# Performance work log

Hardware: AMD Instinct MI355X
Metric: run time of the kernel (lower is better)

The kernel has to match this reference:

```python
import jax, jax.numpy as jnp
import numpy as np

TEMPERATURE = 0.1
EPS = 1e-12  # matches torch F.normalize eps


def _l2_normalize(x, axis=-1):
    n = jnp.sqrt(jnp.sum(x * x, axis=axis, keepdims=True))
    return x / jnp.maximum(n, EPS)


def setup_inputs() -> dict:
    key = jax.random.key(0)
    k1, k2, k3 = jax.random.split(key, 3)
    B, K, D, M = 128, 256, 256, 4
    local_vectors = jax.random.normal(k1, (B, K, D), dtype=jnp.float32)
    prototypes = jax.random.normal(k2, (K * M, D, 1, 1), dtype=jnp.float32)
    concepts_gt = jax.random.randint(k3, (B, K), 0, 2, dtype=jnp.int32)
    return {
        "local_vectors": local_vectors,
        "prototypes": prototypes,
        "concepts_gt": concepts_gt,
        "num_prototypes_per_concept": M,
    }


def reference(local_vectors, prototypes, concepts_gt, num_prototypes_per_concept):
    B, K, D = local_vectors.shape
    M = num_prototypes_per_concept
    protos = prototypes.reshape(K * M, D)  # squeeze(-1).squeeze(-1)
    ln = _l2_normalize(local_vectors)      # (B, K, D)
    pn = _l2_normalize(protos)             # (K*M, D)

    # similarities for every (b, k) query against all prototypes in one GEMM
    sims = jnp.einsum('bkd,pd->bkp', ln, pn) / TEMPERATURE  # (B, K, K*M)

    # logsumexp over all prototypes (shared across the M positives of a concept)
    lse = jax.nn.logsumexp(sims, axis=-1)  # (B, K)

    # sum of positive similarities: prototypes k*M..(k+1)*M-1 for concept k
    # diagonal over the two K axes, summed over m
    pos_sum = jnp.einsum('bkkm->bk', sims.reshape(B, K, K, M))  # (B, K)

    mask = (concepts_gt == 1).astype(sims.dtype)  # (B, K)
    Mf = jnp.asarray(M, sims.dtype)
    total = jnp.sum(mask * (Mf * lse - pos_sum))
    count = Mf * jnp.sum(mask)
    return jnp.where(count > 0, total / jnp.maximum(count, 1.0), jnp.zeros((), sims.dtype))
```

## Files before the change

### kernel.cpp

```cpp
#include <hip/hip_runtime.h>
#include <hip/hip_bf16.h>
#include <stdint.h>

#define KC   256
#define DD   256
#define NPROT 1024
#define NQ   32768

#define OFF_NSEL 0
#define OFF_TOT  8
#define OFF_TICK 16
#define OFF_SEL  256
#define OFF_PN   131328
#define OFF_ACC  655616
#define ACC_STRIDE 32768

#define LN2F    0.69314718055994531f
#define C10L2E  14.426950408889634f

typedef __bf16 bf16x8 __attribute__((ext_vector_type(8)));
typedef float  f32x16 __attribute__((ext_vector_type(16)));

static __device__ __forceinline__ unsigned short f2bf(float x) {
  __hip_bfloat16 h = __float2bfloat16(x);
  return __builtin_bit_cast(unsigned short, h);
}

__global__ __launch_bounds__(256) void prep_k(const float* __restrict__ protos,
                                              unsigned char* __restrict__ ws) {
  if (blockIdx.x == 0 && threadIdx.x == 0) {
    *(int*)(ws + OFF_NSEL)  = 0;
    *(float*)(ws + OFF_TOT) = 0.0f;
    *(int*)(ws + OFF_TICK)  = 0;
  }
  const int w = threadIdx.x >> 6, lane = threadIdx.x & 63;
  const int r = blockIdx.x * 4 + w;
  const float4 v = ((const float4*)protos)[r * 64 + lane];
  float ss = v.x*v.x + v.y*v.y + v.z*v.z + v.w*v.w;
#pragma unroll
  for (int m = 1; m < 64; m <<= 1) ss += __shfl_xor(ss, m, 64);
  const float sc = C10L2E / fmaxf(sqrtf(ss), 1e-12f);
  uint2 p;
  p.x = (unsigned)f2bf(v.x * sc) | ((unsigned)f2bf(v.y * sc) << 16);
  p.y = (unsigned)f2bf(v.z * sc) | ((unsigned)f2bf(v.w * sc) << 16);
  *(uint2*)(ws + OFF_PN + (lane >> 2) * 32768 + r * 32 + (lane & 3) * 8) = p;
}

__global__ __launch_bounds__(256) void compact_k(const int* __restrict__ gt,
                                                 unsigned char* __restrict__ ws) {
  const int idx = blockIdx.x * 256 + threadIdx.x;
  if (gt[idx] == 1) {
    int p = atomicAdd((int*)(ws + OFF_NSEL), 1);
    ((int*)(ws + OFF_SEL))[p] = idx;
  }
}

__global__ __launch_bounds__(256) void main_k(const float* __restrict__ lv,
                                              unsigned char* __restrict__ ws) {
  __shared__ __align__(16) unsigned char Aq[64 * 512];

  const int tid  = threadIdx.x;
  const int w    = tid >> 6;
  const int lane = tid & 63;
  const int hi   = lane >> 5;
  const int l31  = lane & 31;

  const int tile = (int)(blockIdx.x & 511);
  const int c    = (int)(blockIdx.x >> 9);

  const int n_sel = *(const int*)(ws + OFF_NSEL);
  const int base  = tile * 64;
  if (base >= n_sel) return;
  const int* sel = (const int*)(ws + OFF_SEL);

  int valid[2], kqr[2];
#pragma unroll
  for (int j = 0; j < 2; ++j) {
    const int slot = base + j * 32 + l31;
    valid[j] = slot < n_sel;
    const int q = valid[j] ? sel[slot] : sel[base];
    kqr[j] = q & (KC - 1);
  }

  const unsigned char* pn0 = ws + OFF_PN + (c * 256 + w * 64 + l31) * 32 + hi * 16;
  const unsigned char* pn1 = pn0 + 32 * 32;

  bf16x8 pa0[4], pa1[4];
#pragma unroll
  for (int p = 0; p < 4; ++p) {
    pa0[p] = *(const bf16x8*)(pn0 + p * 32768);
    pa1[p] = *(const bf16x8*)(pn1 + p * 32768);
  }

  const int grp = tid >> 4, sub = tid & 15;
#pragma unroll
  for (int t = 0; t < 4; ++t) {
    const int r    = grp * 4 + t;
    const int slot = base + r;
    const int qi   = (slot < n_sel) ? sel[slot] : sel[base];
    float4 vv[4];
#pragma unroll
    for (int u = 0; u < 4; ++u) vv[u] = ((const float4*)lv)[qi * 64 + u * 16 + sub];
    float ss = 0.0f;
#pragma unroll
    for (int u = 0; u < 4; ++u)
      ss += vv[u].x*vv[u].x + vv[u].y*vv[u].y + vv[u].z*vv[u].z + vv[u].w*vv[u].w;
#pragma unroll
    for (int m = 1; m < 16; m <<= 1) ss += __shfl_xor(ss, m, 64);
    const float sc = 1.0f / fmaxf(sqrtf(ss), 1e-12f);
    const int swz = ((r & 7) << 4) ^ (((r >> 3) & 3) << 7);
#pragma unroll
    for (int u = 0; u < 4; ++u) {
      uint2 p;
      p.x = (unsigned)f2bf(vv[u].x * sc) | ((unsigned)f2bf(vv[u].y * sc) << 16);
      p.y = (unsigned)f2bf(vv[u].z * sc) | ((unsigned)f2bf(vv[u].w * sc) << 16);
      *(uint2*)(Aq + r * 512 + ((u * 128 + sub * 8) ^ swz)) = p;
    }
  }
  __syncthreads();

  f32x16 acc[2][2];
#pragma unroll
  for (int i = 0; i < 2; ++i)
#pragma unroll
    for (int j = 0; j < 2; ++j)
#pragma unroll
      for (int t = 0; t < 16; ++t) acc[i][j][t] = 0.0f;

  const int bswz = ((l31 & 7) << 4) ^ (((l31 >> 3) & 3) << 7);

#pragma unroll
  for (int k = 0; k < 16; ++k) {
    const bf16x8 a0 = pa0[k & 3];
    const bf16x8 a1 = pa1[k & 3];
    pa0[k & 3] = *(const bf16x8*)(pn0 + ((k + 4) & 15) * 32768);
    pa1[k & 3] = *(const bf16x8*)(pn1 + ((k + 4) & 15) * 32768);
    const int bc = (k * 32 + hi * 16) ^ bswz;
    const bf16x8 b0 = *(const bf16x8*)(Aq + l31 * 512 + bc);
    const bf16x8 b1 = *(const bf16x8*)(Aq + (32 + l31) * 512 + bc);
    acc[0][0] = __builtin_amdgcn_mfma_f32_32x32x16_bf16(a0, b0, acc[0][0], 0, 0, 0);
    acc[0][1] = __builtin_amdgcn_mfma_f32_32x32x16_bf16(a0, b1, acc[0][1], 0, 0, 0);
    acc[1][0] = __builtin_amdgcn_mfma_f32_32x32x16_bf16(a1, b0, acc[1][0], 0, 0, 0);
    acc[1][1] = __builtin_amdgcn_mfma_f32_32x32x16_bf16(a1, b1, acc[1][1], 0, 0, 0);
  }

  float l_acc[2] = {0.f, 0.f}, p_acc[2] = {0.f, 0.f};
#pragma unroll
  for (int i = 0; i < 2; ++i) {
    const int r4base = c * 64 + w * 16 + i * 8 + hi;
#pragma unroll
    for (int j = 0; j < 2; ++j) {
      float l4[4] = {0.f, 0.f, 0.f, 0.f};
      float p4[4] = {0.f, 0.f, 0.f, 0.f};
#pragma unroll
      for (int g = 0; g < 4; ++g) {
        const float pm = (r4base + 2 * g == kqr[j]) ? 1.0f : 0.0f;
#pragma unroll
        for (int t = 0; t < 4; ++t) {
          const float y = acc[i][j][g * 4 + t];
          l4[t] += __builtin_amdgcn_exp2f(y);
          p4[t] = fmaf(pm, y, p4[t]);
        }
      }
      l_acc[j] += (l4[0] + l4[1]) + (l4[2] + l4[3]);
      p_acc[j] += (p4[0] + p4[1]) + (p4[2] + p4[3]);
    }
  }

#pragma unroll
  for (int j = 0; j < 2; ++j) {
    l_acc[j] += __shfl_xor(l_acc[j], 32, 64);
    p_acc[j] += __shfl_xor(p_acc[j], 32, 64);
  }
  if (hi == 0) {
    float2* accb = (float2*)(ws + OFF_ACC) + (c * 4 + w) * ACC_STRIDE;
#pragma unroll
    for (int j = 0; j < 2; ++j) {
      if (valid[j]) {
        const int slot = base + j * 32 + l31;
        float2 v2; v2.x = l_acc[j]; v2.y = p_acc[j];
        accb[slot] = v2;
      }
    }
  }
}

__global__ __launch_bounds__(256) void finish_k(unsigned char* __restrict__ ws,
                                                float* __restrict__ out) {
  __shared__ float accs[4];
  const int n_sel = *(const int*)(ws + OFF_NSEL);
  const int i = blockIdx.x * 256 + threadIdx.x;
  float contrib = 0.0f;
  if (i < n_sel) {
    const float2* a = (const float2*)(ws + OFF_ACC);
    float L = 0.0f, P = 0.0f;
#pragma unroll
    for (int u = 0; u < 16; ++u) {
      const float2 v = a[u * ACC_STRIDE + i];
      L += v.x; P += v.y;
    }
    contrib = LN2F * (4.0f * __builtin_amdgcn_logf(L) - P);
  }
#pragma unroll
  for (int m = 1; m < 64; m <<= 1) contrib += __shfl_xor(contrib, m, 64);
  if ((threadIdx.x & 63) == 0) accs[threadIdx.x >> 6] = contrib;
  __syncthreads();
  if (threadIdx.x == 0) {
    atomicAdd((float*)(ws + OFF_TOT), (accs[0] + accs[1]) + (accs[2] + accs[3]));
    __threadfence();
    const int t = atomicAdd((int*)(ws + OFF_TICK), 1);
    if (t == 127) {
      const float total = atomicAdd((float*)(ws + OFF_TOT), 0.0f);
      out[0] = (n_sel > 0) ? total / (4.0f * (float)n_sel) : 0.0f;
    }
  }
}

extern "C" void kernel_launch(void* const* d_in, const int* in_sizes, int n_in,
                              void* d_out, int out_size, void* d_ws, size_t ws_size,
                              hipStream_t stream) {
  const float* lv     = (const float*)d_in[0];
  const float* protos = (const float*)d_in[1];
  const int*   gt     = (const int*)d_in[2];
  (void)in_sizes; (void)n_in; (void)out_size; (void)ws_size;
  unsigned char* ws = (unsigned char*)d_ws;

  prep_k<<<256, 256, 0, stream>>>(protos, ws);
  compact_k<<<128, 256, 0, stream>>>(gt, ws);
  main_k<<<2048, 256, 0, stream>>>(lv, ws);
  finish_k<<<128, 256, 0, stream>>>(ws, (float*)d_out);
}
```

Baseline: 41.14 us.

## Precompute normalized bf16 queries once during compaction instead of per tile

```diff
diff --git a/kernel.cpp b/kernel.cpp
--- a/kernel.cpp
+++ b/kernel.cpp
@@ -12,7 +12,9 @@
 #define OFF_TICK 16
 #define OFF_SEL  256
 #define OFF_PN   131328
-#define OFF_ACC  655616
+#define OFF_QN   655616
+#define QSLAB    1048576
+#define OFF_ACC  17432832
 #define ACC_STRIDE 32768
 
 #define LN2F    0.69314718055994531f
@@ -46,17 +48,64 @@
   *(uint2*)(ws + OFF_PN + (lane >> 2) * 32768 + r * 32 + (lane & 3) * 8) = p;
 }
 
-__global__ __launch_bounds__(256) void compact_k(const int* __restrict__ gt,
-                                                 unsigned char* __restrict__ ws) {
-  const int idx = blockIdx.x * 256 + threadIdx.x;
-  if (gt[idx] == 1) {
-    int p = atomicAdd((int*)(ws + OFF_NSEL), 1);
-    ((int*)(ws + OFF_SEL))[p] = idx;
-  }
-}
-
-__global__ __launch_bounds__(256) void main_k(const float* __restrict__ lv,
-                                              unsigned char* __restrict__ ws) {
+__global__ __launch_bounds__(512) void cqn_k(const int* __restrict__ gt,
+                                             const float* __restrict__ lv,
+                                             unsigned char* __restrict__ ws) {
+  __shared__ int wcnt[8], wpre[8];
+  __shared__ int sbase, btot;
+  __shared__ int list[512];
+
+  const int tid  = threadIdx.x;
+  const int wv   = tid >> 6, lane = tid & 63;
+  const int idx  = blockIdx.x * 512 + tid;
+
+  const int selme = (gt[idx] == 1);
+  const unsigned long long bal = __ballot(selme);
+  if (lane == 0) wcnt[wv] = __popcll(bal);
+  __syncthreads();
+  if (tid == 0) {
+    int tot = 0;
+#pragma unroll
+    for (int u = 0; u < 8; ++u) { wpre[u] = tot; tot += wcnt[u]; }
+    btot  = tot;
+    sbase = atomicAdd((int*)(ws + OFF_NSEL), tot);
+  }
+  __syncthreads();
+
+  const int rank = __popcll(bal & ((1ull << lane) - 1ull));
+  if (selme) {
+    const int loc = wpre[wv] + rank;
+    list[loc] = idx;
+    ((int*)(ws + OFF_SEL))[sbase + loc] = idx;
+  }
+  __syncthreads();
+
+  const int grp = tid >> 4, sub = tid & 15;
+  const int nr  = btot, sb = sbase;
+  for (int r = grp; r < nr; r += 32) {
+    const int qi   = list[r];
+    const int slot = sb + r;
+    float4 vv[4];
+#pragma unroll
+    for (int u = 0; u < 4; ++u) vv[u] = ((const float4*)lv)[qi * 64 + u * 16 + sub];
+    float ss = 0.0f;
+#pragma unroll
+    for (int u = 0; u < 4; ++u)
+      ss += vv[u].x*vv[u].x + vv[u].y*vv[u].y + vv[u].z*vv[u].z + vv[u].w*vv[u].w;
+#pragma unroll
+    for (int m = 1; m < 16; m <<= 1) ss += __shfl_xor(ss, m, 64);
+    const float sc = 1.0f / fmaxf(sqrtf(ss), 1e-12f);
+#pragma unroll
+    for (int u = 0; u < 4; ++u) {
+      uint2 p;
+      p.x = (unsigned)f2bf(vv[u].x * sc) | ((unsigned)f2bf(vv[u].y * sc) << 16);
+      p.y = (unsigned)f2bf(vv[u].z * sc) | ((unsigned)f2bf(vv[u].w * sc) << 16);
+      *(uint2*)(ws + OFF_QN + (u * 4 + (sub >> 2)) * QSLAB + slot * 32 + (sub & 3) * 8) = p;
+    }
+  }
+}
+
+__global__ __launch_bounds__(256) void main_k(unsigned char* __restrict__ ws) {
   __shared__ __align__(16) unsigned char Aq[64 * 512];
 
   const int tid  = threadIdx.x;
@@ -92,30 +141,19 @@
     pa1[p] = *(const bf16x8*)(pn1 + p * 32768);
   }
 
-  const int grp = tid >> 4, sub = tid & 15;
-#pragma unroll
-  for (int t = 0; t < 4; ++t) {
-    const int r    = grp * 4 + t;
-    const int slot = base + r;
-    const int qi   = (slot < n_sel) ? sel[slot] : sel[base];
-    float4 vv[4];
-#pragma unroll
-    for (int u = 0; u < 4; ++u) vv[u] = ((const float4*)lv)[qi * 64 + u * 16 + sub];
-    float ss = 0.0f;
-#pragma unroll
-    for (int u = 0; u < 4; ++u)
-      ss += vv[u].x*vv[u].x + vv[u].y*vv[u].y + vv[u].z*vv[u].z + vv[u].w*vv[u].w;
-#pragma unroll
-    for (int m = 1; m < 16; m <<= 1) ss += __shfl_xor(ss, m, 64);
-    const float sc = 1.0f / fmaxf(sqrtf(ss), 1e-12f);
+  const unsigned char* qn = ws + OFF_QN;
+  const int last = n_sel - 1;
+#pragma unroll
+  for (int i = 0; i < 4; ++i) {
+    const int unit = i * 256 + tid;
+    const int s = unit >> 6, r = unit & 63;
+    const int slot = min(base + r, last);
+    const unsigned char* src = qn + s * QSLAB + slot * 32;
+    const uint4 d0 = *(const uint4*)(src);
+    const uint4 d1 = *(const uint4*)(src + 16);
     const int swz = ((r & 7) << 4) ^ (((r >> 3) & 3) << 7);
-#pragma unroll
-    for (int u = 0; u < 4; ++u) {
-      uint2 p;
-      p.x = (unsigned)f2bf(vv[u].x * sc) | ((unsigned)f2bf(vv[u].y * sc) << 16);
-      p.y = (unsigned)f2bf(vv[u].z * sc) | ((unsigned)f2bf(vv[u].w * sc) << 16);
-      *(uint2*)(Aq + r * 512 + ((u * 128 + sub * 8) ^ swz)) = p;
-    }
+    *(uint4*)(Aq + r * 512 + ((s * 32) ^ swz))      = d0;
+    *(uint4*)(Aq + r * 512 + ((s * 32 + 16) ^ swz)) = d1;
   }
   __syncthreads();
 
@@ -226,7 +264,7 @@
   unsigned char* ws = (unsigned char*)d_ws;
 
   prep_k<<<256, 256, 0, stream>>>(protos, ws);
-  compact_k<<<128, 256, 0, stream>>>(gt, ws);
-  main_k<<<2048, 256, 0, stream>>>(lv, ws);
+  cqn_k<<<64, 512, 0, stream>>>(gt, lv, ws);
+  main_k<<<2048, 256, 0, stream>>>(ws);
   finish_k<<<128, 256, 0, stream>>>(ws, (float*)d_out);
 }
```

Measured after the change: 37.82 us. 8.1% less time.
